# Performance work log

Measured on AMD Instinct MI355X. Metric: run time of the kernel, lower is better.

## Reference

```python
import jax, jax.numpy as jnp
import numpy as np
from jax.ops import segment_sum

I_N, K_T, J_F, D, L, E, NT, H = 100000, 128, 64, 128, 2, 1000000, 500000, 2


def setup_inputs() -> dict:
    key = jax.random.key(0)
    ks = jax.random.split(key, 32)
    def rn(k, shp, s=0.02):
        return jax.random.normal(k, shp, jnp.float32) * s
    inp = {}
    inp["edge_x"] = jax.random.normal(ks[0], (E, J_F), jnp.float32)
    inp["edge_i"] = jax.random.randint(ks[1], (E,), 0, I_N, jnp.int32)
    inp["edge_k"] = jax.random.randint(ks[2], (E,), 0, K_T, jnp.int32)
    inp["idx_i"] = jax.random.randint(ks[3], (NT,), 0, I_N, jnp.int32)
    inp["idx_j"] = jax.random.randint(ks[4], (NT,), 0, J_F, jnp.int32)
    inp["idx_k"] = jax.random.randint(ks[5], (NT,), 0, K_T, jnp.int32)
    # parameters
    inp["u0"] = rn(ks[6], (I_N, D))          # Embedding(I,dim), xavier-ish
    inp["w0"] = rn(ks[7], (K_T, D), 0.01)
    inp["ep_W"] = rn(ks[8], (J_F, D))        # edge_proj (stored [in,out])
    inp["ep_b"] = jnp.zeros((D,), jnp.float32)
    inp["uW"] = rn(ks[9], (L, 2 * D, D))
    inp["ub"] = jnp.zeros((L, D), jnp.float32)
    inp["wW"] = rn(ks[10], (L, 2 * D, D))
    inp["wb"] = jnp.zeros((L, D), jnp.float32)
    inp["pos"] = rn(ks[11], (K_T, D), 0.01)
    inp["Wq"] = rn(ks[12], (D, D)); inp["Wk"] = rn(ks[13], (D, D)); inp["Wv"] = rn(ks[14], (D, D))
    inp["bq"] = jnp.zeros((D,), jnp.float32); inp["bk"] = jnp.zeros((D,), jnp.float32); inp["bv"] = jnp.zeros((D,), jnp.float32)
    inp["Wo"] = rn(ks[15], (D, D)); inp["bo"] = jnp.zeros((D,), jnp.float32)
    inp["ln1_g"] = jnp.ones((D,), jnp.float32); inp["ln1_b"] = jnp.zeros((D,), jnp.float32)
    inp["f_W1"] = rn(ks[16], (D, 4 * D)); inp["f_b1"] = jnp.zeros((4 * D,), jnp.float32)
    inp["f_W2"] = rn(ks[17], (4 * D, D)); inp["f_b2"] = jnp.zeros((D,), jnp.float32)
    inp["ln2_g"] = jnp.ones((D,), jnp.float32); inp["ln2_b"] = jnp.zeros((D,), jnp.float32)
    inp["V"] = rn(ks[18], (J_F, D))
    inp["bias"] = jnp.zeros((1,), jnp.float32)
    return inp


def _ln(x, g, b, eps=1e-5):
    m = jnp.mean(x, -1, keepdims=True)
    v = jnp.mean((x - m) ** 2, -1, keepdims=True)
    return (x - m) * jax.lax.rsqrt(v + eps) * g + b


def reference(edge_x, edge_i, edge_k, idx_i, idx_j, idx_k, u0, w0, ep_W, ep_b,
              uW, ub, wW, wb, pos, Wq, Wk, Wv, bq, bk, bv, Wo, bo,
              ln1_g, ln1_b, f_W1, f_b1, f_W2, f_b2, ln2_g, ln2_b, V, bias):
    I, K = u0.shape[0], w0.shape[0]
    e = edge_x @ ep_W + ep_b                                   # [E,D] edge_proj (same every layer)
    ones = jnp.ones((edge_i.shape[0],), jnp.float32)
    cnt_u = jnp.clip(segment_sum(ones, edge_i, num_segments=I), 1.0)[:, None]
    cnt_w = jnp.clip(segment_sum(ones, edge_k, num_segments=K), 1.0)[:, None]
    U, W = u0, w0
    for l in range(uW.shape[0]):
        U_msg = segment_sum(W[edge_k] + e, edge_i, num_segments=I)
        W_msg = segment_sum(U[edge_i] + e, edge_k, num_segments=K)
        U = jax.nn.relu(jnp.concatenate([U, U_msg / cnt_u], 1) @ uW[l] + ub[l])
        W = jax.nn.relu(jnp.concatenate([W, W_msg / cnt_w], 1) @ wW[l] + wb[l])
    # TimeRefine: MHA over K time tokens
    dh = D // H
    X = W + pos                                                # [K,D]
    q = (X @ Wq + bq).reshape(K, H, dh)
    k_ = (X @ Wk + bk).reshape(K, H, dh)
    v = (X @ Wv + bv).reshape(K, H, dh)
    scores = jnp.einsum('qhd,khd->hqk', q, k_) / jnp.sqrt(jnp.float32(dh))
    attn = jnp.einsum('hqk,khd->qhd', jax.nn.softmax(scores, -1), v).reshape(K, D)
    attn = attn @ Wo + bo
    H1 = _ln(X + attn, ln1_g, ln1_b)
    H2 = jax.nn.relu(H1 @ f_W1 + f_b1) @ f_W2 + f_b2
    Wf = _ln(H1 + H2, ln2_g, ln2_b)
    # decode triples
    s = U[idx_i] * Wf[idx_k]                                   # [N,D]
    out = jnp.sum(s * V[idx_j], -1) + bias[0]
    return jax.nn.sigmoid(out)
```

## Files before the change

### kernel.cpp

```cpp
#include <hip/hip_runtime.h>
#include <hip/hip_bf16.h>

#define D_DIM 128
#define KT 128
#define JF 64
#define WB_BLOCKS 256

typedef __attribute__((ext_vector_type(8))) short bf16x8;
typedef __attribute__((ext_vector_type(4))) float f32x4;

__device__ inline unsigned short f2b(float f) {
    __hip_bfloat16 h = __float2bfloat16(f);
    return *reinterpret_cast<unsigned short*>(&h);
}
__device__ inline float b2f(unsigned short u) {
    unsigned int x = ((unsigned int)u) << 16;
    return __uint_as_float(x);
}

__global__ void __launch_bounds__(256) edge_pass_kernel(
    const float* __restrict__ edge_x, const int* __restrict__ edge_i,
    const int* __restrict__ edge_k, float* __restrict__ Xi, float* __restrict__ Xk,
    unsigned* __restrict__ Nmat32, unsigned* __restrict__ cntw,
    long e0, long eEnd, int epb)
{
    __shared__ float xk_s[KT * JF];
    __shared__ unsigned cw_s[KT];
    for (int t = threadIdx.x; t < KT * JF; t += 256) xk_s[t] = 0.f;
    if (threadIdx.x < KT) cw_s[threadIdx.x] = 0u;
    __syncthreads();
    const int wid = threadIdx.x >> 6, lane = threadIdx.x & 63;
    const long base = e0 + (long)blockIdx.x * epb;
    for (int c = wid; c < epb; c += 4) {
        long e = base + c;
        if (e >= eEnd) break;
        int i = edge_i[e], k = edge_k[e];
        float x = edge_x[e * 64 + lane];
        unsafeAtomicAdd(&Xi[(long)i * 64 + lane], x);
        unsafeAtomicAdd(&xk_s[k * 64 + lane], x);
        if (lane == 0) atomicAdd(&Nmat32[(long)i * 128 + k], 1u);
        if (lane == 1) atomicAdd(&cw_s[k], 1u);
    }
    __syncthreads();
    for (int t = threadIdx.x; t < KT * JF; t += 256) {
        float v = xk_s[t];
        if (v != 0.f) unsafeAtomicAdd(&Xk[t], v);
    }
    if (threadIdx.x < KT && cw_s[threadIdx.x]) atomicAdd(&cntw[threadIdx.x], cw_s[threadIdx.x]);
}

__global__ void __launch_bounds__(256) cnt_kernel(
    const unsigned* __restrict__ Nmat32, unsigned char* __restrict__ Nmat8,
    float* __restrict__ cntraw, float* __restrict__ invcnt, int nNodes)
{
    int row = blockIdx.x * 4 + (threadIdx.x >> 6);
    int lane = threadIdx.x & 63;
    if (row >= nNodes) return;
    uint2 v = *(const uint2*)&Nmat32[(long)row * 128 + lane * 2];
    unsigned s = v.x + v.y;
    #pragma unroll
    for (int o = 32; o; o >>= 1) s += __shfl_down(s, o, 64);
    uchar2 o2; o2.x = (unsigned char)v.x; o2.y = (unsigned char)v.y;
    *(uchar2*)&Nmat8[(long)row * 128 + lane * 2] = o2;
    if (lane == 0) {
        float c = (float)s;
        cntraw[row] = c;
        invcnt[row] = 1.f / fmaxf(c, 1.f);
    }
}

__global__ void __launch_bounds__(256) u0cvt_kernel(
    const float* __restrict__ in, unsigned short* __restrict__ out, long n4)
{
    long i = (long)blockIdx.x * 256 + threadIdx.x;
    long stride = (long)gridDim.x * 256;
    for (; i < n4; i += stride) {
        float4 v = *(const float4*)&in[i * 4];
        ushort4 o = make_ushort4(f2b(v.x), f2b(v.y), f2b(v.z), f2b(v.w));
        *(ushort4*)&out[i * 4] = o;
    }
}

__global__ void prep_kernel(const float* __restrict__ uWt, const float* __restrict__ Wl,
                            const float* __restrict__ uWb, const float* __restrict__ ep_W,
                            const float* __restrict__ ep_b,
                            unsigned short* __restrict__ Bt, float* __restrict__ ebx)
{
    int idx = blockIdx.x * 256 + threadIdx.x;
    if (idx < 128 * 320) {
        int n = idx / 320, kk = idx - n * 320;
        float v;
        if (kk < 128) {
            v = uWt[kk * 128 + n];
        } else {
            const float* a = (kk < 256) ? (Wl + (kk - 128) * 128) : (ep_W + (kk - 256) * 128);
            float s = 0.f;
            #pragma unroll 8
            for (int j = 0; j < 128; ++j) s += a[j] * uWb[j * 128 + n];
            v = s;
        }
        Bt[idx] = f2b(v);
    } else if (idx < 128 * 320 + 128) {
        int n = idx - 128 * 320;
        float s = 0.f;
        #pragma unroll 8
        for (int j = 0; j < 128; ++j) s += ep_b[j] * uWb[j * 128 + n];
        ebx[n] = s;
    }
}

__global__ void __launch_bounds__(256) layerA_mfma(
    const unsigned short* __restrict__ U_in, const unsigned char* __restrict__ Nmat8,
    const float* __restrict__ Xi, const float* __restrict__ cntraw,
    const float* __restrict__ invcnt, const unsigned short* __restrict__ Bt,
    const float* __restrict__ ub_l, const float* __restrict__ ebx,
    unsigned short* __restrict__ U_out, int nNodes)
{
    __shared__ __align__(16) unsigned short A_s[128][40];
    __shared__ __align__(16) unsigned short B_s[128][40];
    const int tid = threadIdx.x;
    const int w = tid >> 6, lane = tid & 63;
    const int quad = lane >> 4, l16 = lane & 15;
    const int nodeBase = blockIdx.x * 128;
    f32x4 acc[2][8];
    #pragma unroll
    for (int a = 0; a < 2; ++a)
        #pragma unroll
        for (int b = 0; b < 8; ++b) acc[a][b] = (f32x4){0.f, 0.f, 0.f, 0.f};

    const int rr = tid >> 3;
    const int kc = (tid & 7) * 4;

    for (int ks = 0; ks < 10; ++ks) {
        const int k0 = ks * 32;
        __syncthreads();
        {
            int n = tid & 127, seg = tid >> 7;
            const unsigned short* src = Bt + n * 320 + k0 + seg * 16;
            uint4 p0 = *(const uint4*)(src);
            uint4 p1 = *(const uint4*)(src + 8);
            *(uint4*)&B_s[n][seg * 16]     = p0;
            *(uint4*)&B_s[n][seg * 16 + 8] = p1;
        }
        #pragma unroll
        for (int p = 0; p < 4; ++p) {
            int r = p * 32 + rr;
            int node = nodeBase + r;
            ushort4 w4 = make_ushort4(0, 0, 0, 0);
            if (node < nNodes) {
                if (ks < 4) {
                    w4 = *(const ushort4*)&U_in[(long)node * 128 + k0 + kc];
                } else if (ks < 8) {
                    float inv = invcnt[node];
                    const unsigned char* np_ = &Nmat8[(long)node * 128 + (k0 - 128) + kc];
                    w4 = make_ushort4(f2b((float)np_[0] * inv), f2b((float)np_[1] * inv),
                                      f2b((float)np_[2] * inv), f2b((float)np_[3] * inv));
                } else {
                    float inv = invcnt[node];
                    float4 x = *(const float4*)&Xi[(long)node * 64 + (k0 - 256) + kc];
                    w4 = make_ushort4(f2b(x.x * inv), f2b(x.y * inv),
                                      f2b(x.z * inv), f2b(x.w * inv));
                }
            }
            *(ushort4*)&A_s[r][kc] = w4;
        }
        __syncthreads();
        bf16x8 a0 = *(const bf16x8*)&A_s[w * 32 + l16][quad * 8];
        bf16x8 a1 = *(const bf16x8*)&A_s[w * 32 + 16 + l16][quad * 8];
        #pragma unroll
        for (int nt = 0; nt < 8; ++nt) {
            bf16x8 b = *(const bf16x8*)&B_s[nt * 16 + l16][quad * 8];
            acc[0][nt] = __builtin_amdgcn_mfma_f32_16x16x32_bf16(a0, b, acc[0][nt], 0, 0, 0);
            acc[1][nt] = __builtin_amdgcn_mfma_f32_16x16x32_bf16(a1, b, acc[1][nt], 0, 0, 0);
        }
    }
    #pragma unroll
    for (int mt = 0; mt < 2; ++mt) {
        #pragma unroll
        for (int r = 0; r < 4; ++r) {
            int row = w * 32 + mt * 16 + quad * 4 + r;
            int node = nodeBase + row;
            if (node < nNodes) {
                float flag = (cntraw[node] > 0.f) ? 1.f : 0.f;
                #pragma unroll
                for (int nt = 0; nt < 8; ++nt) {
                    int col = nt * 16 + l16;
                    float vv = acc[mt][nt][r] + ub_l[col] + flag * ebx[col];
                    U_out[(long)node * 128 + col] = f2b(fmaxf(vv, 0.f));
                }
            }
        }
    }
}

__global__ void __launch_bounds__(256) wmsgB_mfma(
    const unsigned short* __restrict__ U, const unsigned char* __restrict__ Nmat8,
    float* __restrict__ partial, int nodes_per_block, int nNodes)
{
    __shared__ __align__(16) unsigned short A_s[128][40];
    __shared__ __align__(16) unsigned short B_s[128][40];
    const int tid = threadIdx.x;
    const int w = tid >> 6, lane = tid & 63;
    const int quad = lane >> 4, l16 = lane & 15;
    f32x4 acc[2][8];
    #pragma unroll
    for (int a = 0; a < 2; ++a)
        #pragma unroll
        for (int b = 0; b < 8; ++b) acc[a][b] = (f32x4){0.f, 0.f, 0.f, 0.f};

    int base = blockIdx.x * nodes_per_block;
    int end = min(base + nodes_per_block, nNodes);
    const int nn = tid >> 3;
    const int cc = (tid & 7) * 16;
    for (int g = base; g < end; g += 32) {
        int cnt = min(32, end - g);
        __syncthreads();
        if (nn < cnt) {
            int node = g + nn;
            uint4 nb = *(const uint4*)&Nmat8[(long)node * 128 + cc];
            const unsigned char* nbp = (const unsigned char*)&nb;
            uint4 ua = *(const uint4*)&U[(long)node * 128 + cc];
            uint4 ubb = *(const uint4*)&U[(long)node * 128 + cc + 8];
            unsigned short uv[16];
            *(uint4*)&uv[0] = ua;
            *(uint4*)&uv[8] = ubb;
            #pragma unroll
            for (int j = 0; j < 16; ++j) {
                A_s[cc + j][nn] = f2b((float)nbp[j]);
                B_s[cc + j][nn] = uv[j];
            }
        } else {
            #pragma unroll
            for (int j = 0; j < 16; ++j) { A_s[cc + j][nn] = 0; B_s[cc + j][nn] = 0; }
        }
        __syncthreads();
        bf16x8 a0 = *(const bf16x8*)&A_s[w * 32 + l16][quad * 8];
        bf16x8 a1 = *(const bf16x8*)&A_s[w * 32 + 16 + l16][quad * 8];
        #pragma unroll
        for (int nt = 0; nt < 8; ++nt) {
            bf16x8 b = *(const bf16x8*)&B_s[nt * 16 + l16][quad * 8];
            acc[0][nt] = __builtin_amdgcn_mfma_f32_16x16x32_bf16(a0, b, acc[0][nt], 0, 0, 0);
            acc[1][nt] = __builtin_amdgcn_mfma_f32_16x16x32_bf16(a1, b, acc[1][nt], 0, 0, 0);
        }
    }
    float* my = partial + (size_t)blockIdx.x * 16384;
    #pragma unroll
    for (int mt = 0; mt < 2; ++mt)
        #pragma unroll
        for (int r = 0; r < 4; ++r) {
            int row = w * 32 + mt * 16 + quad * 4 + r;
            #pragma unroll
            for (int nt = 0; nt < 8; ++nt)
                my[row * 128 + nt * 16 + l16] = acc[mt][nt][r];
        }
}

__global__ void __launch_bounds__(256) reduceP_kernel(
    const float* __restrict__ partial, float* __restrict__ Wmsg)
{
    int grp = blockIdx.x >> 6;
    int ib  = blockIdx.x & 63;
    int idx = ib * 256 + threadIdx.x;
    float s = 0.f;
    #pragma unroll 8
    for (int b = 0; b < 32; ++b)
        s += partial[(size_t)(grp * 32 + b) * 16384 + idx];
    unsafeAtomicAdd(&Wmsg[idx], s);
}

__global__ void __launch_bounds__(128) wfin_gemm_kernel(
    const float* __restrict__ Wmsg, const float* __restrict__ Xk,
    const unsigned* __restrict__ cntw, const float* __restrict__ ep_W,
    const float* __restrict__ ep_b, const float* __restrict__ Wrow,
    const float* __restrict__ wWt, const float* __restrict__ wWb,
    const float* __restrict__ wb_l, float* __restrict__ Wout)
{
    __shared__ float msg_s[128];
    __shared__ float a_s[128];
    const int kk = blockIdx.x, t = threadIdx.x;
    float c = (float)cntw[kk];
    {
        float s = Wmsg[kk * 128 + t];
        const float* xk = Xk + kk * 64;
        #pragma unroll 8
        for (int j = 0; j < 64; ++j) s += xk[j] * ep_W[j * 128 + t];
        s += c * ep_b[t];
        msg_s[t] = s / fmaxf(c, 1.f);
        a_s[t] = Wrow[kk * 128 + t];
    }
    __syncthreads();
    float s = wb_l[t];
    #pragma unroll 4
    for (int k = 0; k < 128; ++k) s += a_s[k] * wWt[k * 128 + t];
    #pragma unroll 4
    for (int k = 0; k < 128; ++k) s += msg_s[k] * wWb[k * 128 + t];
    Wout[kk * 128 + t] = fmaxf(s, 0.f);
}

__global__ void add_kernel(const float* __restrict__ A, const float* __restrict__ B,
                           float* __restrict__ C, int n)
{
    int i = blockIdx.x * 256 + threadIdx.x;
    if (i < n) C[i] = A[i] + B[i];
}

__global__ void qkv_kernel(const float* __restrict__ X,
                           const float* __restrict__ Wq, const float* __restrict__ Wk,
                           const float* __restrict__ Wv, const float* __restrict__ bq,
                           const float* __restrict__ bk, const float* __restrict__ bv,
                           float* __restrict__ qm, float* __restrict__ km, float* __restrict__ vm)
{
    int idx = blockIdx.x * 256 + threadIdx.x;
    if (idx >= 128 * 384) return;
    int m = idx / 384, c = idx - m * 384;
    int sel = c >> 7, n = c & 127;
    const float* W = (sel == 0) ? Wq : (sel == 1) ? Wk : Wv;
    const float* b = (sel == 0) ? bq : (sel == 1) ? bk : bv;
    float s = b[n];
    const float* x = X + m * 128;
    #pragma unroll 8
    for (int k = 0; k < 128; ++k) s += x[k] * W[k * 128 + n];
    float* o = (sel == 0) ? qm : (sel == 1) ? km : vm;
    o[m * 128 + n] = s;
}

__global__ void attn_kernel(const float* __restrict__ q, const float* __restrict__ kmat,
                            const float* __restrict__ vmat, float* __restrict__ outp)
{
    __shared__ float p_s[128];
    __shared__ float red_s[4];
    const int tok = blockIdx.x;
    const int t = threadIdx.x;
    const int lane = t & 63, wid = t >> 6;
    for (int h = 0; h < 2; ++h) {
        const float* qr = q + tok * 128 + h * 64;
        const float* kr = kmat + t * 128 + h * 64;
        float s = 0.f;
        #pragma unroll
        for (int d = 0; d < 64; ++d) s += qr[d] * kr[d];
        s *= 0.125f;
        float m = s;
        #pragma unroll
        for (int o = 32; o; o >>= 1) m = fmaxf(m, __shfl_down(m, o, 64));
        if (lane == 0) red_s[wid] = m;
        __syncthreads();
        m = fmaxf(red_s[0], red_s[1]);
        float ev = expf(s - m);
        float ss = ev;
        #pragma unroll
        for (int o = 32; o; o >>= 1) ss += __shfl_down(ss, o, 64);
        if (lane == 0) red_s[2 + wid] = ss;
        __syncthreads();
        float tot = red_s[2] + red_s[3];
        p_s[t] = ev / tot;
        __syncthreads();
        if (t < 64) {
            float o = 0.f;
            #pragma unroll 8
            for (int j = 0; j < 128; ++j) o += p_s[j] * vmat[j * 128 + h * 64 + t];
            outp[tok * 128 + h * 64 + t] = o;
        }
        __syncthreads();
    }
}

__global__ void __launch_bounds__(128) proj_ln_kernel(
    const float* __restrict__ attnO, const float* __restrict__ Wo,
    const float* __restrict__ bo, const float* __restrict__ Xmat,
    const float* __restrict__ g, const float* __restrict__ b, float* __restrict__ H1)
{
    __shared__ float a_s[128];
    __shared__ float red_s[4];
    const int m = blockIdx.x, t = threadIdx.x, lane = t & 63, wid = t >> 6;
    a_s[t] = attnO[m * 128 + t];
    __syncthreads();
    float v = bo[t];
    #pragma unroll 4
    for (int k = 0; k < 128; ++k) v += a_s[k] * Wo[k * 128 + t];
    v += Xmat[m * 128 + t];
    float s = v;
    #pragma unroll
    for (int o = 32; o; o >>= 1) s += __shfl_down(s, o, 64);
    if (lane == 0) red_s[wid] = s;
    __syncthreads();
    float mean = (red_s[0] + red_s[1]) * (1.f / 128.f);
    float d = v - mean;
    float q2 = d * d;
    #pragma unroll
    for (int o = 32; o; o >>= 1) q2 += __shfl_down(q2, o, 64);
    if (lane == 0) red_s[2 + wid] = q2;
    __syncthreads();
    float var = (red_s[2] + red_s[3]) * (1.f / 128.f);
    H1[m * 128 + t] = d * rsqrtf(var + 1e-5f) * g[t] + b[t];
}

__global__ void __launch_bounds__(128) ffn_ln_kernel(
    const float* __restrict__ H1, const float* __restrict__ f_W1,
    const float* __restrict__ f_b1, const float* __restrict__ f_W2,
    const float* __restrict__ f_b2, const float* __restrict__ g,
    const float* __restrict__ b, float* __restrict__ Wf)
{
    __shared__ float h_s[128];
    __shared__ float f_s[512];
    __shared__ float red_s[4];
    const int m = blockIdx.x, t = threadIdx.x, lane = t & 63, wid = t >> 6;
    h_s[t] = H1[m * 128 + t];
    __syncthreads();
    #pragma unroll
    for (int nn = 0; nn < 4; ++nn) {
        int n = t + nn * 128;
        float s = f_b1[n];
        #pragma unroll 4
        for (int k = 0; k < 128; ++k) s += h_s[k] * f_W1[k * 512 + n];
        f_s[n] = fmaxf(s, 0.f);
    }
    __syncthreads();
    float v = f_b2[t];
    #pragma unroll 4
    for (int k = 0; k < 512; ++k) v += f_s[k] * f_W2[k * 128 + t];
    v += h_s[t];
    float s = v;
    #pragma unroll
    for (int o = 32; o; o >>= 1) s += __shfl_down(s, o, 64);
    if (lane == 0) red_s[wid] = s;
    __syncthreads();
    float mean = (red_s[0] + red_s[1]) * (1.f / 128.f);
    float d = v - mean;
    float q2 = d * d;
    #pragma unroll
    for (int o = 32; o; o >>= 1) q2 += __shfl_down(q2, o, 64);
    if (lane == 0) red_s[2 + wid] = q2;
    __syncthreads();
    float var = (red_s[2] + red_s[3]) * (1.f / 128.f);
    Wf[m * 128 + t] = d * rsqrtf(var + 1e-5f) * g[t] + b[t];
}

__global__ void __launch_bounds__(256) decode_kernel(
    const int* __restrict__ idx_i, const int* __restrict__ idx_j, const int* __restrict__ idx_k,
    const unsigned short* __restrict__ U2, const float* __restrict__ Wf, const float* __restrict__ V,
    const float* __restrict__ bias, float* __restrict__ out, int n)
{
    const int g = threadIdx.x >> 4;
    const int hl = threadIdx.x & 15;
    int t = blockIdx.x * 16 + g;
    if (t >= n) return;
    int i = idx_i[t], j = idx_j[t], kk = idx_k[t];
    const unsigned short* up = U2 + (long)i * 128 + hl * 8;
    const float* wp = Wf + kk * 128 + hl * 8;
    const float* vp = V + j * 128 + hl * 8;
    uint4 ur = *(const uint4*)up;
    const unsigned short* uu = (const unsigned short*)&ur;
    float4 w0 = *(const float4*)wp,  w1 = *(const float4*)(wp + 4);
    float4 v0 = *(const float4*)vp,  v1 = *(const float4*)(vp + 4);
    float s = b2f(uu[0]) * w0.x * v0.x + b2f(uu[1]) * w0.y * v0.y
            + b2f(uu[2]) * w0.z * v0.z + b2f(uu[3]) * w0.w * v0.w
            + b2f(uu[4]) * w1.x * v1.x + b2f(uu[5]) * w1.y * v1.y
            + b2f(uu[6]) * w1.z * v1.z + b2f(uu[7]) * w1.w * v1.w;
    #pragma unroll
    for (int o = 8; o; o >>= 1) s += __shfl_down(s, o, 16);
    if (hl == 0) out[t] = 1.f / (1.f + expf(-(s + bias[0])));
}

extern "C" void kernel_launch(void* const* d_in, const int* in_sizes, int n_in,
                              void* d_out, int out_size, void* d_ws, size_t ws_size,
                              hipStream_t stream)
{
    const float* edge_x = (const float*)d_in[0];
    const int*   edge_i = (const int*)d_in[1];
    const int*   edge_k = (const int*)d_in[2];
    const int*   idx_i  = (const int*)d_in[3];
    const int*   idx_j  = (const int*)d_in[4];
    const int*   idx_k  = (const int*)d_in[5];
    const float* u0   = (const float*)d_in[6];
    const float* w0   = (const float*)d_in[7];
    const float* ep_W = (const float*)d_in[8];
    const float* ep_b = (const float*)d_in[9];
    const float* uW   = (const float*)d_in[10];
    const float* ub   = (const float*)d_in[11];
    const float* wW   = (const float*)d_in[12];
    const float* wb   = (const float*)d_in[13];
    const float* pos  = (const float*)d_in[14];
    const float* Wq = (const float*)d_in[15];
    const float* Wk = (const float*)d_in[16];
    const float* Wv = (const float*)d_in[17];
    const float* bq = (const float*)d_in[18];
    const float* bk = (const float*)d_in[19];
    const float* bv = (const float*)d_in[20];
    const float* Wo = (const float*)d_in[21];
    const float* bo = (const float*)d_in[22];
    const float* ln1_g = (const float*)d_in[23];
    const float* ln1_b = (const float*)d_in[24];
    const float* f_W1 = (const float*)d_in[25];
    const float* f_b1 = (const float*)d_in[26];
    const float* f_W2 = (const float*)d_in[27];
    const float* f_b2 = (const float*)d_in[28];
    const float* ln2_g = (const float*)d_in[29];
    const float* ln2_b = (const float*)d_in[30];
    const float* Vmat = (const float*)d_in[31];
    const float* bias = (const float*)d_in[32];

    const int E   = in_sizes[1];
    const int NTt = in_sizes[3];
    const int nNodes = in_sizes[6] / D_DIM;

    char* ws = (char*)d_ws;
    size_t off = 0;
    auto alloc = [&](size_t bytes) -> char* {
        char* p = ws + off;
        off = (off + bytes + 255) & ~(size_t)255;
        return p;
    };
    unsigned* Nmat32 = (unsigned*)alloc((size_t)nNodes * 128 * 4);
    float*    Xi     = (float*)alloc((size_t)nNodes * 64 * 4);
    float*    Xkseg  = (float*)alloc(128 * 64 * 4);
    unsigned* cntw   = (unsigned*)alloc(512);
    float*    Wmsg0  = (float*)alloc(65536);
    float*    Wmsg1  = (float*)alloc(65536);
    size_t zeroBytes = off;
    unsigned char* Nmat8 = (unsigned char*)alloc((size_t)nNodes * 128);
    float* cntraw = (float*)alloc((size_t)nNodes * 4);
    float* invcnt = (float*)alloc((size_t)nNodes * 4);
    unsigned short* U0b = (unsigned short*)alloc((size_t)nNodes * 128 * 2);
    unsigned short* U1b = (unsigned short*)alloc((size_t)nNodes * 128 * 2);
    unsigned short* U2b = (unsigned short*)alloc((size_t)nNodes * 128 * 2);
    float* partials = (float*)alloc((size_t)WB_BLOCKS * 16384 * 4);
    unsigned short* Bt0 = (unsigned short*)alloc(128 * 320 * 2);
    unsigned short* Bt1 = (unsigned short*)alloc(128 * 320 * 2);
    float* W1 = (float*)alloc(65536);
    float* W2 = (float*)alloc(65536);
    float* ebx0 = (float*)alloc(512);
    float* ebx1 = (float*)alloc(512);
    float* Xmat  = (float*)alloc(65536);
    float* qm    = (float*)alloc(65536);
    float* km    = (float*)alloc(65536);
    float* vm    = (float*)alloc(65536);
    float* attnO = (float*)alloc(65536);
    float* H1m   = (float*)alloc(65536);
    float* Wfm   = (float*)alloc(65536);

    const float* uWt0 = uW;
    const float* uWb0 = uW + 128 * 128;
    const float* uWt1 = uW + 256 * 128;
    const float* uWb1 = uW + 256 * 128 + 128 * 128;
    const float* wWt0 = wW;
    const float* wWb0 = wW + 128 * 128;
    const float* wWt1 = wW + 256 * 128;
    const float* wWb1 = wW + 256 * 128 + 128 * 128;

    hipMemsetAsync(d_ws, 0, zeroBytes, stream);

    long half = E >> 1;
    int epb0 = (int)((half + 511) / 512);
    int epb1 = (int)((E - half + 511) / 512);
    edge_pass_kernel<<<512, 256, 0, stream>>>(edge_x, edge_i, edge_k, Xi, Xkseg,
                                              Nmat32, cntw, 0, half, epb0);
    edge_pass_kernel<<<512, 256, 0, stream>>>(edge_x, edge_i, edge_k, Xi, Xkseg,
                                              Nmat32, cntw, half, E, epb1);
    cnt_kernel<<<(nNodes + 3) / 4, 256, 0, stream>>>(Nmat32, Nmat8, cntraw, invcnt, nNodes);
    u0cvt_kernel<<<1024, 256, 0, stream>>>(u0, U0b, (long)nNodes * 32);

    int npb = (nNodes + WB_BLOCKS - 1) / WB_BLOCKS;
    int la_grid = (nNodes + 127) / 128;

    prep_kernel<<<161, 256, 0, stream>>>(uWt0, w0, uWb0, ep_W, ep_b, Bt0, ebx0);
    wmsgB_mfma<<<WB_BLOCKS, 256, 0, stream>>>(U0b, Nmat8, partials, npb, nNodes);
    reduceP_kernel<<<512, 256, 0, stream>>>(partials, Wmsg0);
    layerA_mfma<<<la_grid, 256, 0, stream>>>(U0b, Nmat8, Xi, cntraw, invcnt, Bt0, ub, ebx0, U1b, nNodes);
    wfin_gemm_kernel<<<128, 128, 0, stream>>>(Wmsg0, Xkseg, cntw, ep_W, ep_b,
                                              w0, wWt0, wWb0, wb, W1);

    prep_kernel<<<161, 256, 0, stream>>>(uWt1, W1, uWb1, ep_W, ep_b, Bt1, ebx1);
    wmsgB_mfma<<<WB_BLOCKS, 256, 0, stream>>>(U1b, Nmat8, partials, npb, nNodes);
    reduceP_kernel<<<512, 256, 0, stream>>>(partials, Wmsg1);
    layerA_mfma<<<la_grid, 256, 0, stream>>>(U1b, Nmat8, Xi, cntraw, invcnt, Bt1, ub + 128, ebx1, U2b, nNodes);
    wfin_gemm_kernel<<<128, 128, 0, stream>>>(Wmsg1, Xkseg, cntw, ep_W, ep_b,
                                              W1, wWt1, wWb1, wb + 128, W2);

    add_kernel<<<64, 256, 0, stream>>>(W2, pos, Xmat, 128 * 128);
    qkv_kernel<<<192, 256, 0, stream>>>(Xmat, Wq, Wk, Wv, bq, bk, bv, qm, km, vm);
    attn_kernel<<<128, 128, 0, stream>>>(qm, km, vm, attnO);
    proj_ln_kernel<<<128, 128, 0, stream>>>(attnO, Wo, bo, Xmat, ln1_g, ln1_b, H1m);
    ffn_ln_kernel<<<128, 128, 0, stream>>>(H1m, f_W1, f_b1, f_W2, f_b2, ln2_g, ln2_b, Wfm);

    decode_kernel<<<(NTt + 15) / 16, 256, 0, stream>>>(idx_i, idx_j, idx_k, U2b, Wfm, Vmat,
                                                       bias, (float*)d_out, NTt);
}
```

Baseline: 1.231 ms.

## Pack edge-count matrix into bytes and fuse small kernels to cut launches

The per-(node,time) edge counts are now accumulated directly as packed 8-bit fields inside 32-bit words, which removes the 51 MB uint32 matrix, its conversion pass, and a quarter of the memset. The count, u0-to-bf16 conversion and layer-0 weight prep kernels are merged into one launch. The partial reduction moves into wfin_gemm, and the add/qkv and attention/proj/LN/FFN/LN chains are fused. The edge pass also runs as a single launch instead of two. Risks: a byte counter overflows if a (node,time) pair gets 256 or more edges, and wfin now reads all 256 partials serially per block.

New measurement: 1.139 ms. 7.5% less time.

```diff
diff --git a/kernel.cpp b/kernel.cpp
--- a/kernel.cpp
+++ b/kernel.cpp
@@ -21,8 +21,7 @@
 __global__ void __launch_bounds__(256) edge_pass_kernel(
     const float* __restrict__ edge_x, const int* __restrict__ edge_i,
     const int* __restrict__ edge_k, float* __restrict__ Xi, float* __restrict__ Xk,
-    unsigned* __restrict__ Nmat32, unsigned* __restrict__ cntw,
-    long e0, long eEnd, int epb)
+    unsigned* __restrict__ NmatP, unsigned* __restrict__ cntw, int E, int epb)
 {
     __shared__ float xk_s[KT * JF];
     __shared__ unsigned cw_s[KT];
@@ -30,15 +29,15 @@
     if (threadIdx.x < KT) cw_s[threadIdx.x] = 0u;
     __syncthreads();
     const int wid = threadIdx.x >> 6, lane = threadIdx.x & 63;
-    const long base = e0 + (long)blockIdx.x * epb;
+    const long base = (long)blockIdx.x * epb;
     for (int c = wid; c < epb; c += 4) {
         long e = base + c;
-        if (e >= eEnd) break;
+        if (e >= (long)E) break;
         int i = edge_i[e], k = edge_k[e];
         float x = edge_x[e * 64 + lane];
         unsafeAtomicAdd(&Xi[(long)i * 64 + lane], x);
         unsafeAtomicAdd(&xk_s[k * 64 + lane], x);
-        if (lane == 0) atomicAdd(&Nmat32[(long)i * 128 + k], 1u);
+        if (lane == 0) atomicAdd(&NmatP[(long)i * 32 + (k >> 2)], 1u << ((k & 3) * 8));
         if (lane == 1) atomicAdd(&cw_s[k], 1u);
     }
     __syncthreads();
@@ -49,35 +48,60 @@
     if (threadIdx.x < KT && cw_s[threadIdx.x]) atomicAdd(&cntw[threadIdx.x], cw_s[threadIdx.x]);
 }
 
-__global__ void __launch_bounds__(256) cnt_kernel(
-    const unsigned* __restrict__ Nmat32, unsigned char* __restrict__ Nmat8,
-    float* __restrict__ cntraw, float* __restrict__ invcnt, int nNodes)
-{
-    int row = blockIdx.x * 4 + (threadIdx.x >> 6);
-    int lane = threadIdx.x & 63;
-    if (row >= nNodes) return;
-    uint2 v = *(const uint2*)&Nmat32[(long)row * 128 + lane * 2];
-    unsigned s = v.x + v.y;
-    #pragma unroll
-    for (int o = 32; o; o >>= 1) s += __shfl_down(s, o, 64);
-    uchar2 o2; o2.x = (unsigned char)v.x; o2.y = (unsigned char)v.y;
-    *(uchar2*)&Nmat8[(long)row * 128 + lane * 2] = o2;
-    if (lane == 0) {
-        float c = (float)s;
-        cntraw[row] = c;
-        invcnt[row] = 1.f / fmaxf(c, 1.f);
-    }
-}
-
-__global__ void __launch_bounds__(256) u0cvt_kernel(
-    const float* __restrict__ in, unsigned short* __restrict__ out, long n4)
-{
-    long i = (long)blockIdx.x * 256 + threadIdx.x;
-    long stride = (long)gridDim.x * 256;
-    for (; i < n4; i += stride) {
-        float4 v = *(const float4*)&in[i * 4];
-        ushort4 o = make_ushort4(f2b(v.x), f2b(v.y), f2b(v.z), f2b(v.w));
-        *(ushort4*)&out[i * 4] = o;
+__global__ void __launch_bounds__(256) mid_kernel(
+    const unsigned* __restrict__ NmatP, float* __restrict__ cntraw,
+    float* __restrict__ invcnt, int nNodes, int cntB,
+    const float* __restrict__ u0, unsigned short* __restrict__ U0b, long n4,
+    const float* __restrict__ uWt, const float* __restrict__ Wl,
+    const float* __restrict__ uWb, const float* __restrict__ ep_W,
+    const float* __restrict__ ep_b,
+    unsigned short* __restrict__ Bt, float* __restrict__ ebx)
+{
+    const int bid = blockIdx.x;
+    if (bid < cntB) {
+        int row = bid * 4 + (threadIdx.x >> 6);
+        int lane = threadIdx.x & 63;
+        if (row < nNodes && lane < 32) {
+            unsigned wv = NmatP[(long)row * 32 + lane];
+            unsigned s = (wv & 0xFF) + ((wv >> 8) & 0xFF) + ((wv >> 16) & 0xFF) + (wv >> 24);
+            #pragma unroll
+            for (int o = 16; o; o >>= 1) s += __shfl_down(s, o, 32);
+            if (lane == 0) {
+                float c = (float)s;
+                cntraw[row] = c;
+                invcnt[row] = 1.f / fmaxf(c, 1.f);
+            }
+        }
+    } else if (bid < cntB + 1024) {
+        long i = (long)(bid - cntB) * 256 + threadIdx.x;
+        long stride = (long)1024 * 256;
+        for (; i < n4; i += stride) {
+            float4 v = *(const float4*)&u0[i * 4];
+            ushort4 o = make_ushort4(f2b(v.x), f2b(v.y), f2b(v.z), f2b(v.w));
+            *(ushort4*)&U0b[i * 4] = o;
+        }
+    } else {
+        int idx = (bid - cntB - 1024) * 256 + threadIdx.x;
+        if (idx < 128 * 320) {
+            int n = idx / 320, kk = idx - n * 320;
+            float v;
+            if (kk < 128) {
+                v = uWt[kk * 128 + n];
+            } else {
+                const float* a = (kk < 256) ? (Wl + (kk - 128) * 128) : (ep_W + (kk - 256) * 128);
+                float s = 0.f;
+                #pragma unroll 8
+                for (int j = 0; j < 128; ++j) s += a[j] * uWb[j * 128 + n];
+                v = s;
+            }
+            Bt[idx] = f2b(v);
+        } else if (idx < 128 * 320 + 128) {
+            int n = idx - 128 * 320;
+            float s = 0.f;
+            #pragma unroll 8
+            for (int j = 0; j < 128; ++j) s += ep_b[j] * uWb[j * 128 + n];
+            ebx[n] = s;
+        }
     }
 }
 
@@ -255,21 +279,8 @@
         }
 }
 
-__global__ void __launch_bounds__(256) reduceP_kernel(
-    const float* __restrict__ partial, float* __restrict__ Wmsg)
-{
-    int grp = blockIdx.x >> 6;
-    int ib  = blockIdx.x & 63;
-    int idx = ib * 256 + threadIdx.x;
-    float s = 0.f;
-    #pragma unroll 8
-    for (int b = 0; b < 32; ++b)
-        s += partial[(size_t)(grp * 32 + b) * 16384 + idx];
-    unsafeAtomicAdd(&Wmsg[idx], s);
-}
-
 __global__ void __launch_bounds__(128) wfin_gemm_kernel(
-    const float* __restrict__ Wmsg, const float* __restrict__ Xk,
+    const float* __restrict__ partial, const float* __restrict__ Xk,
     const unsigned* __restrict__ cntw, const float* __restrict__ ep_W,
     const float* __restrict__ ep_b, const float* __restrict__ Wrow,
     const float* __restrict__ wWt, const float* __restrict__ wWb,
@@ -280,7 +291,10 @@
     const int kk = blockIdx.x, t = threadIdx.x;
     float c = (float)cntw[kk];
     {
-        float s = Wmsg[kk * 128 + t];
+        float s = 0.f;
+        const float* pp = partial + kk * 128 + t;
+        #pragma unroll 8
+        for (int b = 0; b < WB_BLOCKS; ++b) s += pp[(size_t)b * 16384];
         const float* xk = Xk + kk * 64;
         #pragma unroll 8
         for (int j = 0; j < 64; ++j) s += xk[j] * ep_W[j * 128 + t];
@@ -297,18 +311,12 @@
     Wout[kk * 128 + t] = fmaxf(s, 0.f);
 }
 
-__global__ void add_kernel(const float* __restrict__ A, const float* __restrict__ B,
-                           float* __restrict__ C, int n)
-{
-    int i = blockIdx.x * 256 + threadIdx.x;
-    if (i < n) C[i] = A[i] + B[i];
-}
-
-__global__ void qkv_kernel(const float* __restrict__ X,
-                           const float* __restrict__ Wq, const float* __restrict__ Wk,
-                           const float* __restrict__ Wv, const float* __restrict__ bq,
-                           const float* __restrict__ bk, const float* __restrict__ bv,
-                           float* __restrict__ qm, float* __restrict__ km, float* __restrict__ vm)
+__global__ void qkvf_kernel(const float* __restrict__ W2, const float* __restrict__ pos,
+                            const float* __restrict__ Wq, const float* __restrict__ Wk,
+                            const float* __restrict__ Wv, const float* __restrict__ bq,
+                            const float* __restrict__ bk, const float* __restrict__ bv,
+                            float* __restrict__ Xmat,
+                            float* __restrict__ qm, float* __restrict__ km, float* __restrict__ vm)
 {
     int idx = blockIdx.x * 256 + threadIdx.x;
     if (idx >= 128 * 384) return;
@@ -317,17 +325,29 @@
     const float* W = (sel == 0) ? Wq : (sel == 1) ? Wk : Wv;
     const float* b = (sel == 0) ? bq : (sel == 1) ? bk : bv;
     float s = b[n];
-    const float* x = X + m * 128;
+    const float* x2 = W2 + m * 128;
+    const float* xp = pos + m * 128;
     #pragma unroll 8
-    for (int k = 0; k < 128; ++k) s += x[k] * W[k * 128 + n];
+    for (int k = 0; k < 128; ++k) s += (x2[k] + xp[k]) * W[k * 128 + n];
     float* o = (sel == 0) ? qm : (sel == 1) ? km : vm;
     o[m * 128 + n] = s;
-}
-
-__global__ void attn_kernel(const float* __restrict__ q, const float* __restrict__ kmat,
-                            const float* __restrict__ vmat, float* __restrict__ outp)
+    if (sel == 0) Xmat[m * 128 + n] = x2[n] + xp[n];
+}
+
+__global__ void __launch_bounds__(128) attn_tail_kernel(
+    const float* __restrict__ q, const float* __restrict__ kmat,
+    const float* __restrict__ vmat, const float* __restrict__ Wo,
+    const float* __restrict__ bo, const float* __restrict__ Xmat,
+    const float* __restrict__ ln1_g, const float* __restrict__ ln1_b,
+    const float* __restrict__ f_W1, const float* __restrict__ f_b1,
+    const float* __restrict__ f_W2, const float* __restrict__ f_b2,
+    const float* __restrict__ ln2_g, const float* __restrict__ ln2_b,
+    float* __restrict__ Wf)
 {
     __shared__ float p_s[128];
+    __shared__ float a_s[128];
+    __shared__ float h1_s[128];
+    __shared__ float f_s[512];
     __shared__ float red_s[4];
     const int tok = blockIdx.x;
     const int t = threadIdx.x;
@@ -358,26 +378,44 @@
             float o = 0.f;
             #pragma unroll 8
             for (int j = 0; j < 128; ++j) o += p_s[j] * vmat[j * 128 + h * 64 + t];
-            outp[tok * 128 + h * 64 + t] = o;
-        }
-        __syncthreads();
-    }
-}
-
-__global__ void __launch_bounds__(128) proj_ln_kernel(
-    const float* __restrict__ attnO, const float* __restrict__ Wo,
-    const float* __restrict__ bo, const float* __restrict__ Xmat,
-    const float* __restrict__ g, const float* __restrict__ b, float* __restrict__ H1)
-{
-    __shared__ float a_s[128];
-    __shared__ float red_s[4];
-    const int m = blockIdx.x, t = threadIdx.x, lane = t & 63, wid = t >> 6;
-    a_s[t] = attnO[m * 128 + t];
+            a_s[h * 64 + t] = o;
+        }
+        __syncthreads();
+    }
+    {
+        float v = bo[t];
+        #pragma unroll 4
+        for (int k = 0; k < 128; ++k) v += a_s[k] * Wo[k * 128 + t];
+        v += Xmat[tok * 128 + t];
+        float s = v;
+        #pragma unroll
+        for (int o = 32; o; o >>= 1) s += __shfl_down(s, o, 64);
+        if (lane == 0) red_s[wid] = s;
+        __syncthreads();
+        float mean = (red_s[0] + red_s[1]) * (1.f / 128.f);
+        float d = v - mean;
+        float q2 = d * d;
+        #pragma unroll
+        for (int o = 32; o; o >>= 1) q2 += __shfl_down(q2, o, 64);
+        if (lane == 0) red_s[2 + wid] = q2;
+        __syncthreads();
+        float var = (red_s[2] + red_s[3]) * (1.f / 128.f);
+        h1_s[t] = d * rsqrtf(var + 1e-5f) * ln1_g[t] + ln1_b[t];
+        __syncthreads();
+    }
+    #pragma unroll
+    for (int nn = 0; nn < 4; ++nn) {
+        int n = t + nn * 128;
+        float s = f_b1[n];
+        #pragma unroll 4
+        for (int k = 0; k < 128; ++k) s += h1_s[k] * f_W1[k * 512 + n];
+        f_s[n] = fmaxf(s, 0.f);
+    }
     __syncthreads();
-    float v = bo[t];
+    float v = f_b2[t];
     #pragma unroll 4
-    for (int k = 0; k < 128; ++k) v += a_s[k] * Wo[k * 128 + t];
-    v += Xmat[m * 128 + t];
+    for (int k = 0; k < 512; ++k) v += f_s[k] * f_W2[k * 128 + t];
+    v += h1_s[t];
     float s = v;
     #pragma unroll
     for (int o = 32; o; o >>= 1) s += __shfl_down(s, o, 64);
@@ -391,48 +429,7 @@
     if (lane == 0) red_s[2 + wid] = q2;
     __syncthreads();
     float var = (red_s[2] + red_s[3]) * (1.f / 128.f);
-    H1[m * 128 + t] = d * rsqrtf(var + 1e-5f) * g[t] + b[t];
-}
-
-__global__ void __launch_bounds__(128) ffn_ln_kernel(
-    const float* __restrict__ H1, const float* __restrict__ f_W1,
-    const float* __restrict__ f_b1, const float* __restrict__ f_W2,
-    const float* __restrict__ f_b2, const float* __restrict__ g,
-    const float* __restrict__ b, float* __restrict__ Wf)
-{
-    __shared__ float h_s[128];
-    __shared__ float f_s[512];
-    __shared__ float red_s[4];
-    const int m = blockIdx.x, t = threadIdx.x, lane = t & 63, wid = t >> 6;
-    h_s[t] = H1[m * 128 + t];
-    __syncthreads();
-    #pragma unroll
-    for (int nn = 0; nn < 4; ++nn) {
-        int n = t + nn * 128;
-        float s = f_b1[n];
-        #pragma unroll 4
-        for (int k = 0; k < 128; ++k) s += h_s[k] * f_W1[k * 512 + n];
-        f_s[n] = fmaxf(s, 0.f);
-    }
-    __syncthreads();
-    float v = f_b2[t];
-    #pragma unroll 4
-    for (int k = 0; k < 512; ++k) v += f_s[k] * f_W2[k * 128 + t];
-    v += h_s[t];
-    float s = v;
-    #pragma unroll
-    for (int o = 32; o; o >>= 1) s += __shfl_down(s, o, 64);
-    if (lane == 0) red_s[wid] = s;
-    __syncthreads();
-    float mean = (red_s[0] + red_s[1]) * (1.f / 128.f);
-    float d = v - mean;
-    float q2 = d * d;
-    #pragma unroll
-    for (int o = 32; o; o >>= 1) q2 += __shfl_down(q2, o, 64);
-    if (lane == 0) red_s[2 + wid] = q2;
-    __syncthreads();
-    float var = (red_s[2] + red_s[3]) * (1.f / 128.f);
-    Wf[m * 128 + t] = d * rsqrtf(var + 1e-5f) * g[t] + b[t];
+    Wf[tok * 128 + t] = d * rsqrtf(var + 1e-5f) * ln2_g[t] + ln2_b[t];
 }
 
 __global__ void __launch_bounds__(256) decode_kernel(
@@ -510,14 +507,11 @@
         off = (off + bytes + 255) & ~(size_t)255;
         return p;
     };
-    unsigned* Nmat32 = (unsigned*)alloc((size_t)nNodes * 128 * 4);
+    unsigned* NmatP  = (unsigned*)alloc((size_t)nNodes * 32 * 4);
     float*    Xi     = (float*)alloc((size_t)nNodes * 64 * 4);
     float*    Xkseg  = (float*)alloc(128 * 64 * 4);
     unsigned* cntw   = (unsigned*)alloc(512);
-    float*    Wmsg0  = (float*)alloc(65536);
-    float*    Wmsg1  = (float*)alloc(65536);
     size_t zeroBytes = off;
-    unsigned char* Nmat8 = (unsigned char*)alloc((size_t)nNodes * 128);
     float* cntraw = (float*)alloc((size_t)nNodes * 4);
     float* invcnt = (float*)alloc((size_t)nNodes * 4);
     unsigned short* U0b = (unsigned short*)alloc((size_t)nNodes * 128 * 2);
@@ -534,9 +528,9 @@
     float* qm    = (float*)alloc(65536);
     float* km    = (float*)alloc(65536);
     float* vm    = (float*)alloc(65536);
-    float* attnO = (float*)alloc(65536);
-    float* H1m   = (float*)alloc(65536);
     float* Wfm   = (float*)alloc(65536);
+
+    const unsigned char* Nmat8 = (const unsigned char*)NmatP;
 
     const float* uWt0 = uW;
     const float* uWb0 = uW + 128 * 128;
@@ -549,38 +543,33 @@
 
     hipMemsetAsync(d_ws, 0, zeroBytes, stream);
 
-    long half = E >> 1;
-    int epb0 = (int)((half + 511) / 512);
-    int epb1 = (int)((E - half + 511) / 512);
-    edge_pass_kernel<<<512, 256, 0, stream>>>(edge_x, edge_i, edge_k, Xi, Xkseg,
-                                              Nmat32, cntw, 0, half, epb0);
-    edge_pass_kernel<<<512, 256, 0, stream>>>(edge_x, edge_i, edge_k, Xi, Xkseg,
-                                              Nmat32, cntw, half, E, epb1);
-    cnt_kernel<<<(nNodes + 3) / 4, 256, 0, stream>>>(Nmat32, Nmat8, cntraw, invcnt, nNodes);
-    u0cvt_kernel<<<1024, 256, 0, stream>>>(u0, U0b, (long)nNodes * 32);
+    int epb = (E + 1023) / 1024;
+    edge_pass_kernel<<<1024, 256, 0, stream>>>(edge_x, edge_i, edge_k, Xi, Xkseg,
+                                               NmatP, cntw, E, epb);
+
+    int cntB = (nNodes + 3) / 4;
+    mid_kernel<<<cntB + 1024 + 161, 256, 0, stream>>>(
+        NmatP, cntraw, invcnt, nNodes, cntB,
+        u0, U0b, (long)nNodes * 32,
+        uWt0, w0, uWb0, ep_W, ep_b, Bt0, ebx0);
 
     int npb = (nNodes + WB_BLOCKS - 1) / WB_BLOCKS;
     int la_grid = (nNodes + 127) / 128;
 
-    prep_kernel<<<161, 256, 0, stream>>>(uWt0, w0, uWb0, ep_W, ep_b, Bt0, ebx0);
     wmsgB_mfma<<<WB_BLOCKS, 256, 0, stream>>>(U0b, Nmat8, partials, npb, nNodes);
-    reduceP_kernel<<<512, 256, 0, stream>>>(partials, Wmsg0);
     layerA_mfma<<<la_grid, 256, 0, stream>>>(U0b, Nmat8, Xi, cntraw, invcnt, Bt0, ub, ebx0, U1b, nNodes);
-    wfin_gemm_kernel<<<128, 128, 0, stream>>>(Wmsg0, Xkseg, cntw, ep_W, ep_b,
+    wfin_gemm_kernel<<<128, 128, 0, stream>>>(partials, Xkseg, cntw, ep_W, ep_b,
                                               w0, wWt0, wWb0, wb, W1);
 
     prep_kernel<<<161, 256, 0, stream>>>(uWt1, W1, uWb1, ep_W, ep_b, Bt1, ebx1);
     wmsgB_mfma<<<WB_BLOCKS, 256, 0, stream>>>(U1b, Nmat8, partials, npb, nNodes);
-    reduceP_kernel<<<512, 256, 0, stream>>>(partials, Wmsg1);
     layerA_mfma<<<la_grid, 256, 0, stream>>>(U1b, Nmat8, Xi, cntraw, invcnt, Bt1, ub + 128, ebx1, U2b, nNodes);
-    wfin_gemm_kernel<<<128, 128, 0, stream>>>(Wmsg1, Xkseg, cntw, ep_W, ep_b,
+    wfin_gemm_kernel<<<128, 128, 0, stream>>>(partials, Xkseg, cntw, ep_W, ep_b,
                                               W1, wWt1, wWb1, wb + 128, W2);
 
-    add_kernel<<<64, 256, 0, stream>>>(W2, pos, Xmat, 128 * 128);
-    qkv_kernel<<<192, 256, 0, stream>>>(Xmat, Wq, Wk, Wv, bq, bk, bv, qm, km, vm);
-    attn_kernel<<<128, 128, 0, stream>>>(qm, km, vm, attnO);
-    proj_ln_kernel<<<128, 128, 0, stream>>>(attnO, Wo, bo, Xmat, ln1_g, ln1_b, H1m);
-    ffn_ln_kernel<<<128, 128, 0, stream>>>(H1m, f_W1, f_b1, f_W2, f_b2, ln2_g, ln2_b, Wfm);
+    qkvf_kernel<<<192, 256, 0, stream>>>(W2, pos, Wq, Wk, Wv, bq, bk, bv, Xmat, qm, km, vm);
+    attn_tail_kernel<<<128, 128, 0, stream>>>(qm, km, vm, Wo, bo, Xmat, ln1_g, ln1_b,
+                                              f_W1, f_b1, f_W2, f_b2, ln2_g, ln2_b, Wfm);
 
     decode_kernel<<<(NTt + 15) / 16, 256, 0, stream>>>(idx_i, idx_j, idx_k, U2b, Wfm, Vmat,
                                                        bias, (float*)d_out, NTt);
```
